# Kernel optimization log

Measured on AMD Instinct MI355X. Metric: run time of the kernel, lower is better.

The kernel has to match this reference:

```python
import jax, jax.numpy as jnp
import numpy as np

B, N, C, K = 32, 4096, 768, 64

def setup_inputs() -> dict:
    key = jax.random.key(0)
    k1, k2 = jax.random.split(key)
    x = jax.random.normal(k1, (B, N, C), dtype=jnp.float32)
    # nn.Linear(in_dim, K, bias=False) weight has shape [K, in_dim]
    W = jax.random.normal(k2, (K, C), dtype=jnp.float32) * (1.0 / np.sqrt(C))
    return {"x_bhwc": x, "W": W}

def reference(x_bhwc, W):
    # logits: [B, N, K]
    logits = jnp.einsum('bnc,kc->bnk', x_bhwc, W)
    # softmax over spatial dim N (dim=1)
    attn = jax.nn.softmax(logits, axis=1)
    # weighted sum over N -> [B, K, C]
    tokens = jnp.einsum('bnk,bnc->bkc', attn, x_bhwc)
    return tokens
```

## Files before the change

kernel.cpp:

```cpp
#include <hip/hip_runtime.h>
#include <hip/hip_bf16.h>

#define Bdim 32
#define Ndim 4096
#define Cdim 768
#define Kdim 64

typedef float f32x4 __attribute__((ext_vector_type(4)));
typedef short s16x8 __attribute__((ext_vector_type(8)));
typedef __bf16 bf16x8 __attribute__((ext_vector_type(8)));

__device__ __forceinline__ short f2bf(float f) {
  return __builtin_bit_cast(short, (__bf16)f);
}
__device__ __forceinline__ float bf2f(short s) {
  return (float)__builtin_bit_cast(__bf16, s);
}
__device__ __forceinline__ f32x4 MFMA(s16x8 a, s16x8 b, f32x4 c) {
  return __builtin_amdgcn_mfma_f32_16x16x32_bf16(
      __builtin_bit_cast(bf16x8, a), __builtin_bit_cast(bf16x8, b), c, 0, 0, 0);
}

__global__ void k0_wcvt(const float* __restrict__ W, short* __restrict__ Wr) {
  int idx = blockIdx.x * 256 + threadIdx.x;
  if (idx >= Kdim * Cdim / 8) return;
  int k = idx / (Cdim / 8), c8 = idx % (Cdim / 8);
  int cs = c8 >> 2, g = c8 & 3;
  int t = k >> 4, i = k & 15;
  const float* src = W + (size_t)k * Cdim + c8 * 8;
  s16x8 v;
#pragma unroll
  for (int e = 0; e < 8; ++e) v[e] = f2bf(src[e]);
  *(s16x8*)(Wr + ((((size_t)cs * 4 + t) * 4 + g) * 16 + i) * 8) = v;
}

__global__ __launch_bounds__(256) void k1_logits(
    const float* __restrict__ x, const short* __restrict__ Wr,
    short* __restrict__ P, float* __restrict__ ps) {
  const int blk = blockIdx.x;
  const int b = blk >> 6;
  const int ntile = blk & 63;
  const int tid = threadIdx.x;
  const int w = tid >> 6;
  const int l = tid & 63;
  const int g = l >> 4, i = l & 15;

  const float* xrow = x + (size_t)(b * Ndim + ntile * 64 + w * 16 + i) * Cdim;
  f32x4 acc[4] = {};

  for (int grp = 0; grp < 6; ++grp) {
    const int cbase = grp * 128 + g * 8;
    f32x4 xv[8];
    s16x8 wv[4][4];
#pragma unroll
    for (int s = 0; s < 4; ++s) {
      const f32x4* ap = (const f32x4*)(xrow + cbase + s * 32);
      xv[2 * s] = ap[0];
      xv[2 * s + 1] = ap[1];
    }
#pragma unroll
    for (int s = 0; s < 4; ++s) {
#pragma unroll
      for (int t = 0; t < 4; ++t) {
        wv[s][t] = *(const s16x8*)(
            Wr + ((((size_t)(grp * 4 + s) * 4 + t) * 4 + g) * 16 + i) * 8);
      }
    }
#pragma unroll
    for (int s = 0; s < 4; ++s) {
      s16x8 af;
#pragma unroll
      for (int e = 0; e < 4; ++e) af[e] = f2bf(xv[2 * s][e]);
#pragma unroll
      for (int e = 0; e < 4; ++e) af[4 + e] = f2bf(xv[2 * s + 1][e]);
#pragma unroll
      for (int t = 0; t < 4; ++t) acc[t] = MFMA(af, wv[s][t], acc[t]);
    }
  }

  short* Pb = P + (size_t)b * (Ndim * Kdim);
  float sv[4];
#pragma unroll
  for (int t = 0; t < 4; ++t) {
    sv[t] = 0.f;
#pragma unroll
    for (int r = 0; r < 4; ++r) {
      int n = ntile * 64 + w * 16 + g * 4 + r;
      int k = t * 16 + i;
      short hv = f2bf(__expf(acc[t][r]));
      Pb[(n >> 3) * 512 + k * 8 + (n & 7)] = hv;
      sv[t] += bf2f(hv);
    }
    sv[t] += __shfl_xor(sv[t], 16);
    sv[t] += __shfl_xor(sv[t], 32);
  }
  __shared__ float rs[4][4][16];
  if (g == 0) {
#pragma unroll
    for (int t = 0; t < 4; ++t) rs[w][t][i] = sv[t];
  }
  __syncthreads();
  if (w == 0 && g == 0) {
#pragma unroll
    for (int t = 0; t < 4; ++t) {
      float S = rs[0][t][i] + rs[1][t][i] + rs[2][t][i] + rs[3][t][i];
      ps[((size_t)b * 64 + ntile) * 64 + t * 16 + i] = S;
    }
  }
}

__global__ __launch_bounds__(256) void k2b_combine(
    const float* __restrict__ ps, float* __restrict__ invd) {
  const int b = blockIdx.x;
  const int t = threadIdx.x;
  const int k = t & 63, nt4 = t >> 6;
  float S = 0.f;
#pragma unroll
  for (int j = 0; j < 16; ++j)
    S += ps[((size_t)b * 64 + nt4 * 16 + j) * 64 + k];
  __shared__ float ss[4][64];
  ss[nt4][k] = S;
  __syncthreads();
  if (nt4 == 0) {
    float St = ss[0][k] + ss[1][k] + ss[2][k] + ss[3][k];
    invd[b * 64 + k] = 1.f / St;
  }
}

#define CT 48
#define NCH 128
#define NQ 4
__device__ __forceinline__ int swz(int c) {
  return ((((c >> 3) ^ c) & 7) << 4);
}
__global__ __launch_bounds__(256) void k3_tokens(
    const float* __restrict__ x, const short* __restrict__ P,
    float* __restrict__ part) {
  __shared__ short xs[CT * 128];
  char* xsb = (char*)xs;
  const int blk = blockIdx.x;
  const int q = blk & 3;
  const int ct = (blk >> 2) & 15;
  const int b = blk >> 6;
  const int tid = threadIdx.x;
  const int w = tid >> 6, l = tid & 63, g = l >> 4, i = l & 15;

  const float* xb = x + (size_t)b * Ndim * Cdim;
  const short* Pb = P + (size_t)b * (Ndim * Kdim);

  f32x4 acc[3] = {};

#define LOADX(ch, buf)                                                        \
  do {                                                                        \
    const int n0_ = (ch) * NCH;                                               \
    _Pragma("unroll") for (int uu = 0; uu < 3; ++uu) {                        \
      int u_ = tid + uu * 256;                                                \
      int n_ = u_ / 6, c8_ = u_ % 6;                                          \
      const f32x4* src_ =                                                     \
          (const f32x4*)(xb + (size_t)(n0_ + n_) * Cdim + ct * CT + c8_ * 8); \
      buf[uu][0] = src_[0];                                                   \
      buf[uu][1] = src_[1];                                                   \
    }                                                                         \
  } while (0)

#define LOADL(ch, lvb)                                                        \
  do {                                                                        \
    const int nb8_ = (ch) * 16;                                               \
    _Pragma("unroll") for (int ns = 0; ns < 4; ++ns) {                        \
      lvb[ns] = *(const s16x8*)(Pb + (size_t)(nb8_ + ns * 4 + g) * 512 +      \
                                (w * 16 + i) * 8);                            \
    }                                                                         \
  } while (0)

#define STORELDS(buf)                                                         \
  do {                                                                        \
    _Pragma("unroll") for (int uu = 0; uu < 3; ++uu) {                        \
      int u_ = tid + uu * 256;                                                \
      int n_ = u_ / 6, c8_ = u_ % 6;                                          \
      _Pragma("unroll") for (int e = 0; e < 8; ++e) {                         \
        int c_ = c8_ * 8 + e;                                                 \
        float fv_ = (e < 4) ? buf[uu][0][e] : buf[uu][1][e - 4];              \
        *(short*)(xsb + c_ * 256 + ((2 * n_) ^ swz(c_))) = f2bf(fv_);         \
      }                                                                       \
    }                                                                         \
  } while (0)

#define COMPUTE(lvb)                                                          \
  do {                                                                        \
    _Pragma("unroll") for (int ns = 0; ns < 4; ++ns) {                        \
      _Pragma("unroll") for (int cs = 0; cs < 3; ++cs) {                      \
        const int c_ = cs * 16 + i;                                           \
        s16x8 bfr_ = *(const s16x8*)(xsb + c_ * 256 +                         \
                                     ((ns * 64 + g * 16) ^ swz(c_)));         \
        acc[cs] = MFMA(lvb[ns], bfr_, acc[cs]);                               \
      }                                                                       \
    }                                                                         \
  } while (0)

  f32x4 stA[3][2], stB[3][2];
  s16x8 lvA[4], lvB[4];

  const int ch0 = q * 8;
  LOADX(ch0, stA);
  LOADL(ch0, lvA);
  for (int ch = 0; ch < 8; ch += 2) {
    __syncthreads();
    STORELDS(stA);
    LOADX(ch0 + ch + 1, stB);
    LOADL(ch0 + ch + 1, lvB);
    __syncthreads();
    COMPUTE(lvA);
    __syncthreads();
    STORELDS(stB);
    if (ch + 2 < 8) {
      LOADX(ch0 + ch + 2, stA);
      LOADL(ch0 + ch + 2, lvA);
    }
    __syncthreads();
    COMPUTE(lvB);
  }

  float* pb = part + ((size_t)q * Bdim + b) * (Kdim * Cdim);
#pragma unroll
  for (int r = 0; r < 4; ++r) {
    const int k = w * 16 + g * 4 + r;
#pragma unroll
    for (int cs = 0; cs < 3; ++cs) {
      pb[(size_t)k * Cdim + ct * CT + cs * 16 + i] = acc[cs][r];
    }
  }
#undef LOADX
#undef LOADL
#undef STORELDS
#undef COMPUTE
}

#define QSTRIDE (Bdim * Kdim * Cdim / 4)
__global__ __launch_bounds__(256) void k4_reduce(
    const float* __restrict__ part, const float* __restrict__ invd,
    float* __restrict__ out) {
  const int idx = blockIdx.x * 256 + threadIdx.x;
  const f32x4* p = (const f32x4*)part;
  f32x4 s = p[idx] + p[idx + QSTRIDE] + p[idx + 2 * QSTRIDE] + p[idx + 3 * QSTRIDE];
  const float sc = invd[(idx * 4) / Cdim];
  ((f32x4*)out)[idx] = s * sc;
}

extern "C" void kernel_launch(void* const* d_in, const int* in_sizes, int n_in,
                              void* d_out, int out_size, void* d_ws, size_t ws_size,
                              hipStream_t stream) {
  const float* x = (const float*)d_in[0];
  const float* W = (const float*)d_in[1];
  float* out = (float*)d_out;
  char* ws = (char*)d_ws;

  short* Wb = (short*)ws;
  short* P = (short*)(ws + (1 << 17));
  char* after = ws + (1 << 17) + (size_t)Bdim * Ndim * Kdim * 2;
  float* psum = (float*)after;
  float* iv = psum + Bdim * 64 * 64;
  float* part = iv + Bdim * Kdim;

  hipLaunchKernelGGL(k0_wcvt, dim3(24), dim3(256), 0, stream, W, Wb);
  hipLaunchKernelGGL(k1_logits, dim3(Bdim * 64), dim3(256), 0, stream, x, Wb, P, psum);
  hipLaunchKernelGGL(k2b_combine, dim3(Bdim), dim3(256), 0, stream, psum, iv);
  hipLaunchKernelGGL(k3_tokens, dim3(Bdim * 16 * NQ), dim3(256), 0, stream, x, P, part);
  hipLaunchKernelGGL(k4_reduce, dim3(Bdim * Kdim * Cdim / 4 / 256), dim3(256), 0, stream,
                     part, iv, out);
}
```

Before: 211.6 us.

## Double-buffer LDS tile in tokens kernel and halve barriers per chunk

```diff
diff --git a/kernel.cpp b/kernel.cpp
--- a/kernel.cpp
+++ b/kernel.cpp
@@ -130,13 +130,14 @@
 #define CT 48
 #define NCH 128
 #define NQ 4
+#define BUFO (CT * 128)
 __device__ __forceinline__ int swz(int c) {
   return ((((c >> 3) ^ c) & 7) << 4);
 }
 __global__ __launch_bounds__(256) void k3_tokens(
     const float* __restrict__ x, const short* __restrict__ P,
     float* __restrict__ part) {
-  __shared__ short xs[CT * 128];
+  __shared__ short xs[2 * BUFO];
   char* xsb = (char*)xs;
   const int blk = blockIdx.x;
   const int q = blk & 3;
@@ -172,7 +173,7 @@
     }                                                                         \
   } while (0)
 
-#define STORELDS(buf)                                                         \
+#define STORELDS(base, buf)                                                   \
   do {                                                                        \
     _Pragma("unroll") for (int uu = 0; uu < 3; ++uu) {                        \
       int u_ = tid + uu * 256;                                                \
@@ -180,44 +181,52 @@
       _Pragma("unroll") for (int e = 0; e < 8; ++e) {                         \
         int c_ = c8_ * 8 + e;                                                 \
         float fv_ = (e < 4) ? buf[uu][0][e] : buf[uu][1][e - 4];              \
-        *(short*)(xsb + c_ * 256 + ((2 * n_) ^ swz(c_))) = f2bf(fv_);         \
+        *(short*)(xsb + (base) + c_ * 256 + ((2 * n_) ^ swz(c_))) = f2bf(fv_);\
       }                                                                       \
     }                                                                         \
   } while (0)
 
-#define COMPUTE(lvb)                                                          \
+#define COMPUTE(base, lvb)                                                    \
   do {                                                                        \
     _Pragma("unroll") for (int ns = 0; ns < 4; ++ns) {                        \
       _Pragma("unroll") for (int cs = 0; cs < 3; ++cs) {                      \
         const int c_ = cs * 16 + i;                                           \
-        s16x8 bfr_ = *(const s16x8*)(xsb + c_ * 256 +                         \
+        s16x8 bfr_ = *(const s16x8*)(xsb + (base) + c_ * 256 +                \
                                      ((ns * 64 + g * 16) ^ swz(c_)));         \
         acc[cs] = MFMA(lvb[ns], bfr_, acc[cs]);                               \
       }                                                                       \
     }                                                                         \
   } while (0)
 
+#define SOFT_BARRIER()                                                        \
+  do {                                                                        \
+    asm volatile("s_waitcnt lgkmcnt(0)" ::: "memory");                        \
+    __builtin_amdgcn_s_barrier();                                             \
+    __builtin_amdgcn_sched_barrier(0);                                        \
+  } while (0)
+
   f32x4 stA[3][2], stB[3][2];
   s16x8 lvA[4], lvB[4];
 
   const int ch0 = q * 8;
   LOADX(ch0, stA);
   LOADL(ch0, lvA);
-  for (int ch = 0; ch < 8; ch += 2) {
-    __syncthreads();
-    STORELDS(stA);
-    LOADX(ch0 + ch + 1, stB);
-    LOADL(ch0 + ch + 1, lvB);
-    __syncthreads();
-    COMPUTE(lvA);
-    __syncthreads();
-    STORELDS(stB);
-    if (ch + 2 < 8) {
-      LOADX(ch0 + ch + 2, stA);
-      LOADL(ch0 + ch + 2, lvA);
-    }
-    __syncthreads();
-    COMPUTE(lvB);
+  LOADX(ch0 + 1, stB);
+  LOADL(ch0 + 1, lvB);
+  STORELDS(0, stA);
+  SOFT_BARRIER();
+
+  for (int c = 0; c < 8; c += 2) {
+    if (c + 2 < 8) LOADX(ch0 + c + 2, stA);
+    STORELDS(BUFO * 2, stB);
+    COMPUTE(0, lvA);
+    if (c + 2 < 8) LOADL(ch0 + c + 2, lvA);
+    SOFT_BARRIER();
+    if (c + 3 < 8) LOADX(ch0 + c + 3, stB);
+    if (c + 2 < 8) STORELDS(0, stA);
+    COMPUTE(BUFO * 2, lvB);
+    if (c + 3 < 8) LOADL(ch0 + c + 3, lvB);
+    SOFT_BARRIER();
   }
 
   float* pb = part + ((size_t)q * Bdim + b) * (Kdim * Cdim);
@@ -233,6 +242,7 @@
 #undef LOADL
 #undef STORELDS
 #undef COMPUTE
+#undef SOFT_BARRIER
 }
 
 #define QSTRIDE (Bdim * Kdim * Cdim / 4)
```

New measurement: 211.4 us. About the same (-0.1%).
